# Optimization experiments

Hardware: AMD Instinct MI355X
Metric: run time of the kernel (lower is better)

The kernel has to match this reference:

```python
import jax, jax.numpy as jnp
import numpy as np

NUM_LAGS_P1 = 4
N_NODES = 2048


def setup_inputs() -> dict:
    key = jax.random.key(0)
    # Scale so that ||A*A||_1 ~ O(1): entries ~ N(0, s^2), A_sq entries ~ s^2,
    # row sums of A_sq ~ n*s^2. s = 0.02 -> n*s^2 ~ 0.82 for n=2048.
    scale = 0.02
    adjacencies = scale * jax.random.normal(
        key, (NUM_LAGS_P1, N_NODES, N_NODES), dtype=jnp.float32
    )
    return {"adjacencies": adjacencies}


def reference(adjacencies) -> jnp.ndarray:
    # Only the contemporaneous slice A_0 needs the acyclicity constraint.
    A = adjacencies[0]                     # [n, n]
    n = A.shape[0]
    A_sq = A * A                           # elementwise square (NOTEARS h(A))
    E = jax.scipy.linalg.expm(A_sq)        # Pade + scaling-and-squaring
    h = jnp.trace(E) - n                   # scalar constraint value
    return h
```

## Files before the change

kernel.cpp:

```cpp
#include <hip/hip_runtime.h>
#include <hip/hip_bf16.h>

#define NN 2048
typedef unsigned short us;
typedef __attribute__((ext_vector_type(8))) short short8;
typedef __attribute__((ext_vector_type(4))) float f4;
typedef __attribute__((ext_vector_type(4))) float f32x4;
typedef __attribute__((ext_vector_type(8))) unsigned short us8;

__device__ __forceinline__ us f2bf(float f) {
    unsigned int u = __float_as_uint(f);
    u += 0x7fffu + ((u >> 16) & 1u);
    return (us)(u >> 16);
}
__device__ __forceinline__ float bf2f(us h) {
    return __uint_as_float(((unsigned int)h) << 16);
}
__device__ __forceinline__ void gload16(const us* g, us* l) {
    __builtin_amdgcn_global_load_lds(
        (const __attribute__((address_space(1))) unsigned int*)g,
        (__attribute__((address_space(3))) unsigned int*)l, 16, 0, 0);
}
__device__ __forceinline__ void pair_decode(int b, int& I, int& J) {
    I = 0;
    while (b >= 32 - I) { b -= 32 - I; ++I; }
    J = I + b;
}

__global__ void prep_kernel(const float* __restrict__ A0,
                            us* __restrict__ Bbf, us* __restrict__ BbfT,
                            double* __restrict__ pt1, double* __restrict__ pt2) {
    __shared__ float sIJ[64][65], sJI[64][65];
    __shared__ double wred[2][4];
    int I, J; pair_decode(blockIdx.x, I, J);
    const bool diag = (I == J);
    const int tid = threadIdx.x, lane = tid & 63, wv = tid >> 6;
    const size_t rI = (size_t)I * 64, rJ = (size_t)J * 64;

    #pragma unroll
    for (int u = tid; u < 512; u += 256) {
        const int row = u >> 3, c8 = (u & 7) * 8;
        f4 a0 = *(const f4*)&A0[(rI + row) * NN + rJ + c8];
        f4 a1 = *(const f4*)&A0[(rI + row) * NN + rJ + c8 + 4];
        us8 o;
        #pragma unroll
        for (int k = 0; k < 4; ++k) { float s = a0[k]*a0[k]; sIJ[row][c8+k] = s; o[k] = f2bf(s); }
        #pragma unroll
        for (int k = 0; k < 4; ++k) { float s = a1[k]*a1[k]; sIJ[row][c8+4+k] = s; o[4+k] = f2bf(s); }
        *(us8*)&Bbf[(rI + row) * NN + rJ + c8] = o;
        if (!diag) {
            f4 b0 = *(const f4*)&A0[(rJ + row) * NN + rI + c8];
            f4 b1 = *(const f4*)&A0[(rJ + row) * NN + rI + c8 + 4];
            us8 p;
            #pragma unroll
            for (int k = 0; k < 4; ++k) { float s = b0[k]*b0[k]; sJI[row][c8+k] = s; p[k] = f2bf(s); }
            #pragma unroll
            for (int k = 0; k < 4; ++k) { float s = b1[k]*b1[k]; sJI[row][c8+4+k] = s; p[4+k] = f2bf(s); }
            *(us8*)&Bbf[(rJ + row) * NN + rI + c8] = p;
        }
    }
    __syncthreads();

    #pragma unroll
    for (int u = tid; u < 512; u += 256) {
        const int r = u & 63, c0 = (u >> 6) * 8;
        us8 o;
        #pragma unroll
        for (int k = 0; k < 8; ++k) o[k] = f2bf(sIJ[c0 + k][r]);
        *(us8*)&BbfT[(rJ + r) * NN + rI + c0] = o;
        if (!diag) {
            us8 p;
            #pragma unroll
            for (int k = 0; k < 8; ++k) p[k] = f2bf(sJI[c0 + k][r]);
            *(us8*)&BbfT[(rI + r) * NN + rJ + c0] = p;
        }
    }

    double t1 = 0, t2 = 0;
    for (int rr = wv; rr < 64; rr += 4) {
        float sij = sIJ[rr][lane];
        float sji = diag ? sIJ[lane][rr] : sJI[lane][rr];
        if (diag) { t2 += (double)sij * sji; if (rr == lane) t1 += sij; }
        else       t2 += 2.0 * (double)sij * sji;
    }
    #pragma unroll
    for (int s = 32; s > 0; s >>= 1) {
        t1 += __shfl_down(t1, s, 64);
        t2 += __shfl_down(t2, s, 64);
    }
    if (lane == 0) { wred[0][wv] = t1; wred[1][wv] = t2; }
    __syncthreads();
    if (tid == 0) {
        pt1[blockIdx.x] = wred[0][0] + wred[0][1] + wred[0][2] + wred[0][3];
        pt2[blockIdx.x] = wred[1][0] + wred[1][1] + wred[1][2] + wred[1][3];
    }
}

__launch_bounds__(256, 2)
__global__ void gemm_kernel(const us* __restrict__ A, const us* __restrict__ BT,
                            us* __restrict__ c2a, us* __restrict__ c2b,
                            float* __restrict__ rs, float* __restrict__ cs) {
    __shared__ us lA[2][4096];
    __shared__ us lB[2][4096];
    const int tid  = threadIdx.x;
    const int lane = tid & 63;
    const int w    = tid >> 6;
    const int wr   = w >> 1, wc = w & 1;
    const int rowBase = blockIdx.y * 128;
    const int colBase = blockIdx.x * 128;
    const int kbase   = blockIdx.z * 1024;
    us* __restrict__ C = blockIdx.z ? c2b : c2a;
    const int lr = lane & 15;
    const int lk = (lane >> 4) * 8;

    const int srow = tid >> 2;
    const int scol = (tid & 3) * 8;
    const us* gA0 = A  + (size_t)(rowBase + srow) * NN + kbase + scol;
    const us* gA1 = A  + (size_t)(rowBase + 64 + srow) * NN + kbase + scol;
    const us* gB0 = BT + (size_t)(colBase + srow) * NN + kbase + scol;
    const us* gB1 = BT + (size_t)(colBase + 64 + srow) * NN + kbase + scol;
    const int d0 = srow * 32 + scol;
    const int d1 = (64 + srow) * 32 + scol;

    f32x4 acc[4][4] = {};

    gload16(gA0, &lA[0][d0]);
    gload16(gA1, &lA[0][d1]);
    gload16(gB0, &lB[0][d0]);
    gload16(gB1, &lB[0][d1]);
    __syncthreads();

    for (int t = 0; t < 32; ++t) {
        const int cur = t & 1;
        if (t < 31) {
            const int k = (t + 1) * 32;
            gload16(gA0 + k, &lA[cur ^ 1][d0]);
            gload16(gA1 + k, &lA[cur ^ 1][d1]);
            gload16(gB0 + k, &lB[cur ^ 1][d0]);
            gload16(gB1 + k, &lB[cur ^ 1][d1]);
        }
        short8 af[4], bfr[4];
        #pragma unroll
        for (int mi = 0; mi < 4; ++mi)
            af[mi] = *(const short8*)&lA[cur][(wr * 64 + mi * 16 + lr) * 32 + lk];
        #pragma unroll
        for (int ni = 0; ni < 4; ++ni)
            bfr[ni] = *(const short8*)&lB[cur][(wc * 64 + ni * 16 + lr) * 32 + lk];
        #pragma unroll
        for (int mi = 0; mi < 4; ++mi)
            #pragma unroll
            for (int ni = 0; ni < 4; ++ni)
                acc[mi][ni] = __builtin_amdgcn_mfma_f32_16x16x32_bf16(
                    af[mi], bfr[ni], acc[mi][ni], 0, 0, 0);
        __syncthreads();
    }

    const int orow = (lane >> 4) * 4;
    const int ocol = lane & 15;
    float colp[4] = {0.f, 0.f, 0.f, 0.f};
    #pragma unroll
    for (int mi = 0; mi < 4; ++mi) {
        #pragma unroll
        for (int r = 0; r < 4; ++r) {
            const int gr = rowBase + wr * 64 + mi * 16 + orow + r;
            float rowp = 0.f;
            #pragma unroll
            for (int ni = 0; ni < 4; ++ni) {
                float v = acc[mi][ni][r];
                C[(size_t)gr * NN + colBase + wc * 64 + ni * 16 + ocol] = f2bf(v);
                rowp += v;
                colp[ni] += v;
            }
            rowp += __shfl_xor(rowp, 1, 64);
            rowp += __shfl_xor(rowp, 2, 64);
            rowp += __shfl_xor(rowp, 4, 64);
            rowp += __shfl_xor(rowp, 8, 64);
            if ((lane & 15) == 0) atomicAdd(&rs[gr], rowp);
        }
    }
    #pragma unroll
    for (int ni = 0; ni < 4; ++ni) {
        colp[ni] += __shfl_xor(colp[ni], 16, 64);
        colp[ni] += __shfl_xor(colp[ni], 32, 64);
        if (lane < 16) atomicAdd(&cs[colBase + wc * 64 + ni * 16 + ocol], colp[ni]);
    }
}

__global__ void corr_kernel(const us* __restrict__ c2a, const us* __restrict__ c2b,
                            const us* __restrict__ BbfT,
                            double* __restrict__ pt3, double* __restrict__ pt4) {
    __shared__ float cIJ[64][65], cJI[64][65];
    __shared__ double wred[2][4];
    int I, J; pair_decode(blockIdx.x, I, J);
    const bool diag = (I == J);
    const int tid = threadIdx.x, lane = tid & 63, wv = tid >> 6;
    const size_t rI = (size_t)I * 64, rJ = (size_t)J * 64;

    double t3 = 0;
    #pragma unroll
    for (int u = tid; u < 512; u += 256) {
        const int row = u >> 3, c8 = (u & 7) * 8;
        const size_t off = (rI + row) * NN + rJ + c8;
        us8 va = *(const us8*)&c2a[off];
        us8 vb = *(const us8*)&c2b[off];
        us8 vt = *(const us8*)&BbfT[off];
        #pragma unroll
        for (int k = 0; k < 8; ++k) {
            float c = bf2f(va[k]) + bf2f(vb[k]);
            cIJ[row][c8 + k] = c;
            t3 += (double)(c * bf2f(vt[k]));
        }
        if (!diag) {
            const size_t off2 = (rJ + row) * NN + rI + c8;
            us8 wa = *(const us8*)&c2a[off2];
            us8 wb = *(const us8*)&c2b[off2];
            us8 wt = *(const us8*)&BbfT[off2];
            #pragma unroll
            for (int k = 0; k < 8; ++k) {
                float c = bf2f(wa[k]) + bf2f(wb[k]);
                cJI[row][c8 + k] = c;
                t3 += (double)(c * bf2f(wt[k]));
            }
        }
    }
    __syncthreads();

    double t4 = 0;
    for (int rr = wv; rr < 64; rr += 4) {
        float a = cIJ[rr][lane];
        float b = diag ? cIJ[lane][rr] : cJI[lane][rr];
        t4 += (double)a * b;
    }
    if (!diag) t4 *= 2.0;

    #pragma unroll
    for (int s = 32; s > 0; s >>= 1) {
        t3 += __shfl_down(t3, s, 64);
        t4 += __shfl_down(t4, s, 64);
    }
    if (lane == 0) { wred[0][wv] = t3; wred[1][wv] = t4; }
    __syncthreads();
    if (tid == 0) {
        pt3[blockIdx.x] = wred[0][0] + wred[0][1] + wred[0][2] + wred[0][3];
        pt4[blockIdx.x] = wred[1][0] + wred[1][1] + wred[1][2] + wred[1][3];
    }
}

__global__ void finalize_kernel(const float* __restrict__ rs,
                                const float* __restrict__ cs,
                                const double* __restrict__ pt1,
                                const double* __restrict__ pt2,
                                const double* __restrict__ pt3,
                                const double* __restrict__ pt4,
                                float* __restrict__ out) {
    __shared__ double red[256];
    const int t = threadIdx.x;
    double t1 = 0, t2 = 0, t3 = 0, t4 = 0, s2 = 0, s4 = 0;
    for (int i = t; i < 528; i += 256) {
        t1 += pt1[i]; t2 += pt2[i]; t3 += pt3[i]; t4 += pt4[i];
    }
    for (int i = t; i < NN; i += 256) {
        double r = rs[i];
        s2 += r; s4 += r * (double)cs[i];
    }
    double vals[6] = {t1, t2, t3, t4, s2, s4};
    double tot[6];
    for (int v = 0; v < 6; ++v) {
        red[t] = vals[v]; __syncthreads();
        for (int s = 128; s > 0; s >>= 1) { if (t < s) red[t] += red[t + s]; __syncthreads(); }
        tot[v] = red[0]; __syncthreads();
    }
    if (t == 0) {
        double lam2 = tot[5] / tot[4];
        double lam  = sqrt(lam2);
        double tail = exp(lam) - 1.0 - lam - lam2 * 0.5
                      - lam * lam2 * (1.0 / 6.0) - lam2 * lam2 * (1.0 / 24.0);
        out[0] = (float)(tot[0] + tot[1] * 0.5 + tot[2] * (1.0 / 6.0)
                         + tot[3] * (1.0 / 24.0) + tail);
    }
}

extern "C" void kernel_launch(void* const* d_in, const int* in_sizes, int n_in,
                              void* d_out, int out_size, void* d_ws, size_t ws_size,
                              hipStream_t stream) {
    const float* A0 = (const float*)d_in[0];
    char* ws = (char*)d_ws;
    us*     Bbf  = (us*)(ws);
    us*     BbfT = (us*)(ws + 8388608);
    us*     c2a  = (us*)(ws + 16777216);
    us*     c2b  = (us*)(ws + 25165824);
    float*  rs   = (float*)(ws + 33554432);
    float*  cs   = (float*)(ws + 33562624);
    double* pt1  = (double*)(ws + 33570816);
    double* pt2  = (double*)(ws + 33579008);
    double* pt3  = (double*)(ws + 33587200);
    double* pt4  = (double*)(ws + 33595392);
    float*  out  = (float*)d_out;

    hipMemsetAsync(ws + 33554432, 0, 16384, stream);
    prep_kernel<<<528, 256, 0, stream>>>(A0, Bbf, BbfT, pt1, pt2);
    gemm_kernel<<<dim3(16, 16, 2), 256, 0, stream>>>(Bbf, BbfT, c2a, c2b, rs, cs);
    corr_kernel<<<528, 256, 0, stream>>>(c2a, c2b, BbfT, pt3, pt4);
    finalize_kernel<<<1, 256, 0, stream>>>(rs, cs, pt1, pt2, pt3, pt4, out);
}
```

Baseline: 143.1 us.

## Use full 32x32 tile grids for prep/corr, drop memset, move trace(B^2) to corr

The prep and correction kernels move from a 528-block upper-triangular pair decomposition, where off-diagonal blocks do double work, to a uniform 32x32 grid with one tile per block. The loop-based pair decode and the warp divergence between diagonal and off-diagonal blocks go away. The trace(B^2) partial now comes from the bf16 B and B^T in corr_kernel rather than fp32 squares in prep. The rs/cs memset is replaced by zeroing inside the diagonal prep blocks, which removes one launch. The trade-off is more blocks, some redundant global reads in corr, and t2 now summed in bf16 precision.

Measured after the change: 139.5 us. 2.5% less time.

```diff
diff --git a/kernel.cpp b/kernel.cpp
--- a/kernel.cpp
+++ b/kernel.cpp
@@ -21,19 +21,13 @@
         (const __attribute__((address_space(1))) unsigned int*)g,
         (__attribute__((address_space(3))) unsigned int*)l, 16, 0, 0);
 }
-__device__ __forceinline__ void pair_decode(int b, int& I, int& J) {
-    I = 0;
-    while (b >= 32 - I) { b -= 32 - I; ++I; }
-    J = I + b;
-}
 
 __global__ void prep_kernel(const float* __restrict__ A0,
                             us* __restrict__ Bbf, us* __restrict__ BbfT,
-                            double* __restrict__ pt1, double* __restrict__ pt2) {
-    __shared__ float sIJ[64][65], sJI[64][65];
-    __shared__ double wred[2][4];
-    int I, J; pair_decode(blockIdx.x, I, J);
-    const bool diag = (I == J);
+                            float* __restrict__ rs, float* __restrict__ cs,
+                            double* __restrict__ pt1) {
+    __shared__ float sq[64][65];
+    const int I = blockIdx.y, J = blockIdx.x;
     const int tid = threadIdx.x, lane = tid & 63, wv = tid >> 6;
     const size_t rI = (size_t)I * 64, rJ = (size_t)J * 64;
 
@@ -44,55 +38,30 @@
         f4 a1 = *(const f4*)&A0[(rI + row) * NN + rJ + c8 + 4];
         us8 o;
         #pragma unroll
-        for (int k = 0; k < 4; ++k) { float s = a0[k]*a0[k]; sIJ[row][c8+k] = s; o[k] = f2bf(s); }
-        #pragma unroll
-        for (int k = 0; k < 4; ++k) { float s = a1[k]*a1[k]; sIJ[row][c8+4+k] = s; o[4+k] = f2bf(s); }
+        for (int k = 0; k < 4; ++k) { float s = a0[k] * a0[k]; sq[row][c8 + k] = s; o[k] = f2bf(s); }
+        #pragma unroll
+        for (int k = 0; k < 4; ++k) { float s = a1[k] * a1[k]; sq[row][c8 + 4 + k] = s; o[4 + k] = f2bf(s); }
         *(us8*)&Bbf[(rI + row) * NN + rJ + c8] = o;
-        if (!diag) {
-            f4 b0 = *(const f4*)&A0[(rJ + row) * NN + rI + c8];
-            f4 b1 = *(const f4*)&A0[(rJ + row) * NN + rI + c8 + 4];
-            us8 p;
+    }
+    __syncthreads();
+
+    #pragma unroll
+    for (int u = tid; u < 512; u += 256) {
+        const int r = u >> 3, c0 = (u & 7) * 8;
+        us8 o;
+        #pragma unroll
+        for (int k = 0; k < 8; ++k) o[k] = f2bf(sq[c0 + k][r]);
+        *(us8*)&BbfT[(rJ + r) * NN + rI + c0] = o;
+    }
+
+    if (I == J) {
+        if (tid < 64) { rs[rI + tid] = 0.f; cs[rI + tid] = 0.f; }
+        if (wv == 0) {
+            double t1 = sq[lane][lane];
             #pragma unroll
-            for (int k = 0; k < 4; ++k) { float s = b0[k]*b0[k]; sJI[row][c8+k] = s; p[k] = f2bf(s); }
-            #pragma unroll
-            for (int k = 0; k < 4; ++k) { float s = b1[k]*b1[k]; sJI[row][c8+4+k] = s; p[4+k] = f2bf(s); }
-            *(us8*)&Bbf[(rJ + row) * NN + rI + c8] = p;
-        }
-    }
-    __syncthreads();
-
-    #pragma unroll
-    for (int u = tid; u < 512; u += 256) {
-        const int r = u & 63, c0 = (u >> 6) * 8;
-        us8 o;
-        #pragma unroll
-        for (int k = 0; k < 8; ++k) o[k] = f2bf(sIJ[c0 + k][r]);
-        *(us8*)&BbfT[(rJ + r) * NN + rI + c0] = o;
-        if (!diag) {
-            us8 p;
-            #pragma unroll
-            for (int k = 0; k < 8; ++k) p[k] = f2bf(sJI[c0 + k][r]);
-            *(us8*)&BbfT[(rI + r) * NN + rJ + c0] = p;
-        }
-    }
-
-    double t1 = 0, t2 = 0;
-    for (int rr = wv; rr < 64; rr += 4) {
-        float sij = sIJ[rr][lane];
-        float sji = diag ? sIJ[lane][rr] : sJI[lane][rr];
-        if (diag) { t2 += (double)sij * sji; if (rr == lane) t1 += sij; }
-        else       t2 += 2.0 * (double)sij * sji;
-    }
-    #pragma unroll
-    for (int s = 32; s > 0; s >>= 1) {
-        t1 += __shfl_down(t1, s, 64);
-        t2 += __shfl_down(t2, s, 64);
-    }
-    if (lane == 0) { wred[0][wv] = t1; wred[1][wv] = t2; }
-    __syncthreads();
-    if (tid == 0) {
-        pt1[blockIdx.x] = wred[0][0] + wred[0][1] + wred[0][2] + wred[0][3];
-        pt2[blockIdx.x] = wred[1][0] + wred[1][1] + wred[1][2] + wred[1][3];
+            for (int s = 32; s > 0; s >>= 1) t1 += __shfl_down(t1, s, 64);
+            if (lane == 0) pt1[I] = t1;
+        }
     }
 }
 
@@ -187,62 +156,63 @@
 }
 
 __global__ void corr_kernel(const us* __restrict__ c2a, const us* __restrict__ c2b,
-                            const us* __restrict__ BbfT,
-                            double* __restrict__ pt3, double* __restrict__ pt4) {
-    __shared__ float cIJ[64][65], cJI[64][65];
-    __shared__ double wred[2][4];
-    int I, J; pair_decode(blockIdx.x, I, J);
-    const bool diag = (I == J);
+                            const us* __restrict__ Bbf, const us* __restrict__ BbfT,
+                            double* __restrict__ pt2, double* __restrict__ pt3,
+                            double* __restrict__ pt4) {
+    __shared__ float cT[64][65];
+    __shared__ double wred[3][4];
+    const int I = blockIdx.y, J = blockIdx.x;
     const int tid = threadIdx.x, lane = tid & 63, wv = tid >> 6;
     const size_t rI = (size_t)I * 64, rJ = (size_t)J * 64;
 
-    double t3 = 0;
-    #pragma unroll
-    for (int u = tid; u < 512; u += 256) {
+    double t2 = 0, t3 = 0;
+    float myC[2][8];
+    #pragma unroll
+    for (int ph = 0; ph < 2; ++ph) {
+        const int u = tid + ph * 256;
         const int row = u >> 3, c8 = (u & 7) * 8;
-        const size_t off = (rI + row) * NN + rJ + c8;
+        const size_t off  = (rI + row) * NN + rJ + c8;
+        const size_t off2 = (rJ + row) * NN + rI + c8;
         us8 va = *(const us8*)&c2a[off];
         us8 vb = *(const us8*)&c2b[off];
         us8 vt = *(const us8*)&BbfT[off];
+        us8 vf = *(const us8*)&Bbf[off];
+        us8 wa = *(const us8*)&c2a[off2];
+        us8 wb = *(const us8*)&c2b[off2];
         #pragma unroll
         for (int k = 0; k < 8; ++k) {
             float c = bf2f(va[k]) + bf2f(vb[k]);
-            cIJ[row][c8 + k] = c;
+            myC[ph][k] = c;
             t3 += (double)(c * bf2f(vt[k]));
-        }
-        if (!diag) {
-            const size_t off2 = (rJ + row) * NN + rI + c8;
-            us8 wa = *(const us8*)&c2a[off2];
-            us8 wb = *(const us8*)&c2b[off2];
-            us8 wt = *(const us8*)&BbfT[off2];
-            #pragma unroll
-            for (int k = 0; k < 8; ++k) {
-                float c = bf2f(wa[k]) + bf2f(wb[k]);
-                cJI[row][c8 + k] = c;
-                t3 += (double)(c * bf2f(wt[k]));
-            }
+            t2 += (double)(bf2f(vf[k]) * bf2f(vt[k]));
+            cT[row][c8 + k] = bf2f(wa[k]) + bf2f(wb[k]);
         }
     }
     __syncthreads();
 
     double t4 = 0;
-    for (int rr = wv; rr < 64; rr += 4) {
-        float a = cIJ[rr][lane];
-        float b = diag ? cIJ[lane][rr] : cJI[lane][rr];
-        t4 += (double)a * b;
-    }
-    if (!diag) t4 *= 2.0;
+    #pragma unroll
+    for (int ph = 0; ph < 2; ++ph) {
+        const int u = tid + ph * 256;
+        const int row = u >> 3, c8 = (u & 7) * 8;
+        #pragma unroll
+        for (int k = 0; k < 8; ++k)
+            t4 += (double)(myC[ph][k] * cT[c8 + k][row]);
+    }
 
     #pragma unroll
     for (int s = 32; s > 0; s >>= 1) {
+        t2 += __shfl_down(t2, s, 64);
         t3 += __shfl_down(t3, s, 64);
         t4 += __shfl_down(t4, s, 64);
     }
-    if (lane == 0) { wred[0][wv] = t3; wred[1][wv] = t4; }
+    if (lane == 0) { wred[0][wv] = t2; wred[1][wv] = t3; wred[2][wv] = t4; }
     __syncthreads();
     if (tid == 0) {
-        pt3[blockIdx.x] = wred[0][0] + wred[0][1] + wred[0][2] + wred[0][3];
-        pt4[blockIdx.x] = wred[1][0] + wred[1][1] + wred[1][2] + wred[1][3];
+        const int b = blockIdx.y * 32 + blockIdx.x;
+        pt2[b] = wred[0][0] + wred[0][1] + wred[0][2] + wred[0][3];
+        pt3[b] = wred[1][0] + wred[1][1] + wred[1][2] + wred[1][3];
+        pt4[b] = wred[2][0] + wred[2][1] + wred[2][2] + wred[2][3];
     }
 }
 
@@ -256,9 +226,8 @@
     __shared__ double red[256];
     const int t = threadIdx.x;
     double t1 = 0, t2 = 0, t3 = 0, t4 = 0, s2 = 0, s4 = 0;
-    for (int i = t; i < 528; i += 256) {
-        t1 += pt1[i]; t2 += pt2[i]; t3 += pt3[i]; t4 += pt4[i];
-    }
+    if (t < 32) t1 = pt1[t];
+    for (int i = t; i < 1024; i += 256) { t2 += pt2[i]; t3 += pt3[i]; t4 += pt4[i]; }
     for (int i = t; i < NN; i += 256) {
         double r = rs[i];
         s2 += r; s4 += r * (double)cs[i];
@@ -292,14 +261,13 @@
     float*  rs   = (float*)(ws + 33554432);
     float*  cs   = (float*)(ws + 33562624);
     double* pt1  = (double*)(ws + 33570816);
-    double* pt2  = (double*)(ws + 33579008);
-    double* pt3  = (double*)(ws + 33587200);
-    double* pt4  = (double*)(ws + 33595392);
+    double* pt2  = (double*)(ws + 33571328);
+    double* pt3  = (double*)(ws + 33579520);
+    double* pt4  = (double*)(ws + 33587712);
     float*  out  = (float*)d_out;
 
-    hipMemsetAsync(ws + 33554432, 0, 16384, stream);
-    prep_kernel<<<528, 256, 0, stream>>>(A0, Bbf, BbfT, pt1, pt2);
+    prep_kernel<<<dim3(32, 32), 256, 0, stream>>>(A0, Bbf, BbfT, rs, cs, pt1);
     gemm_kernel<<<dim3(16, 16, 2), 256, 0, stream>>>(Bbf, BbfT, c2a, c2b, rs, cs);
-    corr_kernel<<<528, 256, 0, stream>>>(c2a, c2b, BbfT, pt3, pt4);
+    corr_kernel<<<dim3(32, 32), 256, 0, stream>>>(c2a, c2b, Bbf, BbfT, pt2, pt3, pt4);
     finalize_kernel<<<1, 256, 0, stream>>>(rs, cs, pt1, pt2, pt3, pt4, out);
 }
```
